# Kernel tuning notes

Hardware: AMD Instinct MI355X
Metric: run time of the kernel (lower is better)

## Reference

```python
import jax, jax.numpy as jnp
import numpy as np

BN_EPS = 1e-5


def _binarize_act(x):
    # sign(x) forward, clipped STE backward (grad passes where |x|<1)
    xc = jnp.clip(x, -1.0, 1.0)
    return xc + jax.lax.stop_gradient(jnp.sign(x) - xc)


def _binarize_weight(w):
    # XNOR/ReActNet: per-out-channel scale * sign(w); clipped-STE gradient
    scale = jax.lax.stop_gradient(jnp.mean(jnp.abs(w), axis=(1, 2, 3), keepdims=True))
    wc = jnp.clip(w, -1.0, 1.0)
    return wc + jax.lax.stop_gradient(scale * jnp.sign(w) - wc)


def setup_inputs() -> dict:
    key = jax.random.key(0)
    ks = jax.random.split(key, 8)
    B, C, H, W = 64, 64, 56, 56
    P = 64  # planes == inplanes (stride 1, no downsample)
    x = jax.random.normal(ks[0], (B, C, H, W), dtype=jnp.float32)
    bias0 = jnp.zeros((1, C, 1, 1), dtype=jnp.float32)
    w = jax.random.normal(ks[1], (P, C, 3, 3), dtype=jnp.float32) * 0.1
    gamma = jnp.ones((P,), dtype=jnp.float32)
    beta = jnp.zeros((P,), dtype=jnp.float32)
    run_mean = jax.random.normal(ks[2], (P,), dtype=jnp.float32) * 0.1
    run_var = jax.random.uniform(ks[3], (P,), dtype=jnp.float32, minval=0.5, maxval=1.5)
    bias1 = jnp.zeros((1, P, 1, 1), dtype=jnp.float32)
    alpha = jnp.full((P,), 0.25, dtype=jnp.float32)  # PReLU default init
    bias2 = jnp.zeros((1, P, 1, 1), dtype=jnp.float32)
    return {"x": x, "bias0": bias0, "w": w, "gamma": gamma, "beta": beta,
            "run_mean": run_mean, "run_var": run_var, "bias1": bias1,
            "alpha": alpha, "bias2": bias2}


def reference(x, bias0, w, gamma, beta, run_mean, run_var, bias1, alpha, bias2):
    residual = x
    out = x + bias0                      # move0 (LearnableBias)
    out = _binarize_act(out)             # BinAct: sign, clipped STE
    bw = _binarize_weight(w)             # BinConv weight binarization
    out = jax.lax.conv_general_dilated(
        out, bw, window_strides=(1, 1), padding=((1, 1), (1, 1)),
        dimension_numbers=("NCHW", "OIHW", "NCHW"))
    # BatchNorm2d (inference form with running stats)
    inv = gamma / jnp.sqrt(run_var + BN_EPS)
    out = out * inv[None, :, None, None] + (beta - run_mean * inv)[None, :, None, None]
    out = out + residual                 # residual add (downsample is None)
    out = out + bias1                    # move1
    a = alpha[None, :, None, None]
    out = jnp.where(out >= 0, out, a * out)  # PReLU
    out = out + bias2                    # move2
    return out
```

## Files before the change

### kernel.cpp

```cpp
#include <hip/hip_runtime.h>

typedef unsigned long long u64;

#define BATCH 64
#define CH    64
#define HH    56
#define WW    56
#define HW    3136
#define NBAND 14
#define NBLK  (BATCH * NBAND)

__global__ __launch_bounds__(256)
void fold_kernel(const float* __restrict__ w,
                 const float* __restrict__ gamma,
                 const float* __restrict__ beta,
                 const float* __restrict__ rmean,
                 const float* __restrict__ rvar,
                 const float* __restrict__ bias1,
                 const float* __restrict__ alpha,
                 const float* __restrict__ bias2,
                 u64* __restrict__ wbits,
                 float* __restrict__ kc,
                 float4* __restrict__ c4) {
    __shared__ float red[4];
    const int tid = threadIdx.x;
    const int lane = tid & 63;
    const int wv = tid >> 6;
    const int p = blockIdx.x;
    const float* wp = w + p * 576;

    float s = 0.f;
    for (int i = tid; i < 576; i += 256) s += fabsf(wp[i]);
#pragma unroll
    for (int off = 32; off > 0; off >>= 1) s += __shfl_down(s, off);
    if (lane == 0) red[wv] = s;
    __syncthreads();

    u64 m[9];
    if (wv == 0) {
#pragma unroll
        for (int t = 0; t < 9; ++t) {
            m[t] = __ballot(wp[lane * 9 + t] > 0.f);
            if (lane == 0) wbits[p * 10 + t] = m[t];
        }
        if (lane == 0) wbits[p * 10 + 9] = 0;
    }
    if (tid == 0) {
        float scale = (red[0] + red[1] + red[2] + red[3]) * (1.0f / 576.0f);
        float inv = gamma[p] * rsqrtf(rvar[p] + 1e-5f);
        float am = scale * inv;
        float bd = beta[p] - rmean[p] * inv + bias1[p];
        float pt[9];
#pragma unroll
        for (int t = 0; t < 9; ++t) pt[t] = (float)__popcll(m[t]);
        const float cL = pt[0] + pt[3] + pt[6];
        const float cR = pt[2] + pt[5] + pt[8];
        const float rT = pt[0] + pt[1] + pt[2];
        const float rB = pt[6] + pt[7] + pt[8];
        float Ci[3][3] = {
            {0.f, cL,                 cR},
            {rT,  rT + pt[3] + pt[6], rT + pt[5] + pt[8]},
            {rB,  rB + pt[0] + pt[3], rB + pt[2] + pt[5]}};
        float nv[3][3] = {{9, 6, 6}, {6, 4, 4}, {6, 4, 4}};
#pragma unroll
        for (int wc = 0; wc < 3; ++wc)
#pragma unroll
            for (int lc = 0; lc < 3; ++lc)
                kc[wc * 192 + lc * 64 + p] =
                    fmaf(am, 64.f * nv[wc][lc] + 2.f * Ci[wc][lc], bd);
        c4[p] = make_float4(-2.f * am, alpha[p], bias2[p], 0.f);
    }
}

__global__ __launch_bounds__(512, 6)
void fused_kernel(const float* __restrict__ x,
                  const float* __restrict__ bias0,
                  const u64* __restrict__ wbits,
                  const float* __restrict__ kc,
                  const float4* __restrict__ c4,
                  float* __restrict__ out) {
    __shared__ __align__(16) u64 Lsgn[6][58];
    __shared__ __align__(16) u64 wsm[64 * 10];
    __shared__ float kcsm[576];
    __shared__ float4 c4sm[64];

    const int tid = threadIdx.x;
    const int lane = tid & 63;
    const int wv = tid >> 6;

    for (int i = tid; i < 640; i += 512) wsm[i] = wbits[i];
    for (int i = tid; i < 576; i += 512) kcsm[i] = kc[i];
    if (tid < 64) c4sm[tid] = c4[tid];

    const int bid = blockIdx.x;
    const int wg = (bid & 7) * 112 + (bid >> 3);
    const int b = wg / NBAND;
    const int band = wg - b * NBAND;
    const int r0 = band * 4;

    if (wv < 6) {
        const int ir = r0 - 1 + wv;
        const bool rowok = (unsigned)ir < (unsigned)HH;
        u64 mine = 0;
        if (rowok) {
            const float* xp = x + ((size_t)(b * CH + lane)) * HW + ir * WW;
            const float bz = bias0[lane];
#pragma unroll
            for (int q = 0; q < 14; ++q) {
                float4 v = *(const float4*)(xp + q * 4);
                u64 m0 = __ballot(v.x + bz > 0.f);
                u64 m1 = __ballot(v.y + bz > 0.f);
                u64 m2 = __ballot(v.z + bz > 0.f);
                u64 m3 = __ballot(v.w + bz > 0.f);
                mine = (lane == q * 4 + 0) ? m0 : mine;
                mine = (lane == q * 4 + 1) ? m1 : mine;
                mine = (lane == q * 4 + 2) ? m2 : mine;
                mine = (lane == q * 4 + 3) ? m3 : mine;
            }
        }
        if (lane < WW) Lsgn[wv][1 + lane] = mine;
        else if (lane == 56) Lsgn[wv][0] = 0;
        else if (lane == 57) Lsgn[wv][57] = 0;
    }
    __syncthreads();

    const int rl = wv & 3;
    const int ph = (wv >> 2) << 5;
    const int h = r0 + rl;
    const int wcol = min(lane, WW - 1);
    const bool active = lane < WW;

    u64 a[9];
#pragma unroll
    for (int t = 0; t < 9; ++t)
        a[t] = Lsgn[rl + t / 3][wcol + t % 3];

    const int wclass = (h == 0) ? 1 : (h == HH - 1) ? 2 : 0;
    const int lclass = (wcol == 0) ? 1 : (lane == WW - 1) ? 2 : 0;
    const float* kp = kcsm + wclass * 192 + lclass * 64;

    const size_t xbase = (size_t)b * CH * HW + (size_t)h * WW + wcol;

#pragma unroll 4
    for (int i = 0; i < 32; ++i) {
        const int p = ph + i;
        const u64* wp = wsm + p * 10;
        unsigned int P = 0;
#pragma unroll
        for (int t = 0; t < 9; ++t) {
            u64 v = a[t] ^ wp[t];
            P += __popc((unsigned int)v);
            P += __popc((unsigned int)(v >> 32));
        }
        const float4 cc = c4sm[p];
        const float k = kp[p];
        const size_t off = xbase + (size_t)p * HW;
        const float res = x[off];
        float v = fmaf(cc.x, (float)P, k) + res;
        v = v >= 0.f ? v : cc.y * v;
        v += cc.z;
        if (active) out[off] = v;
    }
}

extern "C" void kernel_launch(void* const* d_in, const int* in_sizes, int n_in,
                              void* d_out, int out_size, void* d_ws, size_t ws_size,
                              hipStream_t stream) {
    const float* x     = (const float*)d_in[0];
    const float* bias0 = (const float*)d_in[1];
    const float* w     = (const float*)d_in[2];
    const float* gamma = (const float*)d_in[3];
    const float* beta  = (const float*)d_in[4];
    const float* rmean = (const float*)d_in[5];
    const float* rvar  = (const float*)d_in[6];
    const float* bias1 = (const float*)d_in[7];
    const float* alpha = (const float*)d_in[8];
    const float* bias2 = (const float*)d_in[9];
    float* out = (float*)d_out;

    char* ws = (char*)d_ws;
    u64* wbits = (u64*)ws;
    float* kc  = (float*)(ws + 5120);
    float4* c4 = (float4*)(ws + 8192);

    fold_kernel<<<64, 256, 0, stream>>>(
        w, gamma, beta, rmean, rvar, bias1, alpha, bias2, wbits, kc, c4);

    fused_kernel<<<NBLK, 512, 0, stream>>>(x, bias0, wbits, kc, c4, out);
}
```

Baseline: 48.38 us.

## Read packed weight table via scalar loads and prefetch residuals in a ring

Packs the weight sign bits and per-channel epilogue constants into one 12-word record per output channel. The fused kernel now reads that record straight from global memory through a wave-uniform pointer (readfirstlane), which allows scalar loads, instead of staging it in LDS. The residual x values are prefetched 8 channels ahead in a register ring, and the 32-iteration loop is fully unrolled with 32-bit offsets. This aims to cut LDS traffic and hide the latency of the residual loads, at the cost of higher register pressure.

Result: no change. 49.03 us (+1.4%).

```diff
diff --git a/kernel.cpp b/kernel.cpp
--- a/kernel.cpp
+++ b/kernel.cpp
@@ -1,6 +1,7 @@
 #include <hip/hip_runtime.h>
 
 typedef unsigned long long u64;
+typedef unsigned int u32;
 
 #define BATCH 64
 #define CH    64
@@ -19,9 +20,8 @@
                  const float* __restrict__ bias1,
                  const float* __restrict__ alpha,
                  const float* __restrict__ bias2,
-                 u64* __restrict__ wbits,
-                 float* __restrict__ kc,
-                 float4* __restrict__ c4) {
+                 u64* __restrict__ wtab,
+                 float* __restrict__ kc) {
     __shared__ float red[4];
     const int tid = threadIdx.x;
     const int lane = tid & 63;
@@ -36,61 +36,60 @@
     if (lane == 0) red[wv] = s;
     __syncthreads();
 
-    u64 m[9];
     if (wv == 0) {
+        u64 m[9];
 #pragma unroll
         for (int t = 0; t < 9; ++t) {
             m[t] = __ballot(wp[lane * 9 + t] > 0.f);
-            if (lane == 0) wbits[p * 10 + t] = m[t];
+            if (lane == 0) wtab[p * 12 + t] = m[t];
         }
-        if (lane == 0) wbits[p * 10 + 9] = 0;
-    }
-    if (tid == 0) {
-        float scale = (red[0] + red[1] + red[2] + red[3]) * (1.0f / 576.0f);
-        float inv = gamma[p] * rsqrtf(rvar[p] + 1e-5f);
-        float am = scale * inv;
-        float bd = beta[p] - rmean[p] * inv + bias1[p];
-        float pt[9];
-#pragma unroll
-        for (int t = 0; t < 9; ++t) pt[t] = (float)__popcll(m[t]);
-        const float cL = pt[0] + pt[3] + pt[6];
-        const float cR = pt[2] + pt[5] + pt[8];
-        const float rT = pt[0] + pt[1] + pt[2];
-        const float rB = pt[6] + pt[7] + pt[8];
-        float Ci[3][3] = {
-            {0.f, cL,                 cR},
-            {rT,  rT + pt[3] + pt[6], rT + pt[5] + pt[8]},
-            {rB,  rB + pt[0] + pt[3], rB + pt[2] + pt[5]}};
-        float nv[3][3] = {{9, 6, 6}, {6, 4, 4}, {6, 4, 4}};
-#pragma unroll
-        for (int wc = 0; wc < 3; ++wc)
-#pragma unroll
-            for (int lc = 0; lc < 3; ++lc)
-                kc[wc * 192 + lc * 64 + p] =
-                    fmaf(am, 64.f * nv[wc][lc] + 2.f * Ci[wc][lc], bd);
-        c4[p] = make_float4(-2.f * am, alpha[p], bias2[p], 0.f);
+        if (lane == 0) {
+            float scale = (red[0] + red[1] + red[2] + red[3]) * (1.0f / 576.0f);
+            float inv = gamma[p] * rsqrtf(rvar[p] + 1e-5f);
+            float am = scale * inv;
+            float bd = beta[p] - rmean[p] * inv + bias1[p];
+            float pt[9];
+#pragma unroll
+            for (int t = 0; t < 9; ++t) pt[t] = (float)__popcll(m[t]);
+            const float cL = pt[0] + pt[3] + pt[6];
+            const float cR = pt[2] + pt[5] + pt[8];
+            const float rT = pt[0] + pt[1] + pt[2];
+            const float rB = pt[6] + pt[7] + pt[8];
+            float Ci[3][3] = {
+                {0.f, cL,                 cR},
+                {rT,  rT + pt[3] + pt[6], rT + pt[5] + pt[8]},
+                {rB,  rB + pt[0] + pt[3], rB + pt[2] + pt[5]}};
+            float nv[3][3] = {{9, 6, 6}, {6, 4, 4}, {6, 4, 4}};
+#pragma unroll
+            for (int wc = 0; wc < 3; ++wc)
+#pragma unroll
+                for (int lc = 0; lc < 3; ++lc)
+                    kc[(wc * 3 + lc) * 64 + p] =
+                        fmaf(am, 64.f * nv[wc][lc] + 2.f * Ci[wc][lc], bd);
+            float* cf = (float*)(wtab + p * 12 + 9);
+            cf[0] = -2.f * am;
+            cf[1] = alpha[p];
+            cf[2] = bias2[p];
+            cf[3] = 0.f;
+            wtab[p * 12 + 11] = 0;
+        }
     }
 }
 
 __global__ __launch_bounds__(512, 6)
 void fused_kernel(const float* __restrict__ x,
                   const float* __restrict__ bias0,
-                  const u64* __restrict__ wbits,
+                  const u64* __restrict__ wtab,
                   const float* __restrict__ kc,
-                  const float4* __restrict__ c4,
                   float* __restrict__ out) {
     __shared__ __align__(16) u64 Lsgn[6][58];
-    __shared__ __align__(16) u64 wsm[64 * 10];
     __shared__ float kcsm[576];
-    __shared__ float4 c4sm[64];
 
     const int tid = threadIdx.x;
     const int lane = tid & 63;
     const int wv = tid >> 6;
 
-    for (int i = tid; i < 640; i += 512) wsm[i] = wbits[i];
     for (int i = tid; i < 576; i += 512) kcsm[i] = kc[i];
-    if (tid < 64) c4sm[tid] = c4[tid];
 
     const int bid = blockIdx.x;
     const int wg = (bid & 7) * 112 + (bid >> 3);
@@ -118,48 +117,60 @@
                 mine = (lane == q * 4 + 3) ? m3 : mine;
             }
         }
-        if (lane < WW) Lsgn[wv][1 + lane] = mine;
-        else if (lane == 56) Lsgn[wv][0] = 0;
-        else if (lane == 57) Lsgn[wv][57] = 0;
+        if (lane < WW)        Lsgn[wv][1 + lane] = mine;
+        else if (lane == 56)  Lsgn[wv][0] = 0;
+        else if (lane == 57)  Lsgn[wv][57] = 0;
     }
     __syncthreads();
 
     const int rl = wv & 3;
-    const int ph = (wv >> 2) << 5;
+    const int ph = __builtin_amdgcn_readfirstlane((wv >> 2) << 5);
     const int h = r0 + rl;
-    const int wcol = min(lane, WW - 1);
+    const int wl = min(lane, WW - 1);
     const bool active = lane < WW;
 
     u64 a[9];
 #pragma unroll
     for (int t = 0; t < 9; ++t)
-        a[t] = Lsgn[rl + t / 3][wcol + t % 3];
+        a[t] = Lsgn[rl + t / 3][wl + t % 3];
 
     const int wclass = (h == 0) ? 1 : (h == HH - 1) ? 2 : 0;
-    const int lclass = (wcol == 0) ? 1 : (lane == WW - 1) ? 2 : 0;
-    const float* kp = kcsm + wclass * 192 + lclass * 64;
-
-    const size_t xbase = (size_t)b * CH * HW + (size_t)h * WW + wcol;
-
-#pragma unroll 4
+    const int lclass = (lane == 0) ? 1 : (lane == WW - 1) ? 2 : 0;
+    const float* kp = kcsm + (wclass * 3 + lclass) * 64 + ph;
+
+    u32 off = (u32)(b * CH * HW + h * WW + wl) + (u32)ph * HW;
+    const u64* wp = wtab + ph * 12;
+
+    float res[8];
+#pragma unroll
+    for (int j = 0; j < 8; ++j) res[j] = x[off + (u32)j * HW];
+
+#pragma unroll
     for (int i = 0; i < 32; ++i) {
-        const int p = ph + i;
-        const u64* wp = wsm + p * 10;
-        unsigned int P = 0;
-#pragma unroll
-        for (int t = 0; t < 9; ++t) {
-            u64 v = a[t] ^ wp[t];
-            P += __popc((unsigned int)v);
-            P += __popc((unsigned int)(v >> 32));
-        }
-        const float4 cc = c4sm[p];
-        const float k = kp[p];
-        const size_t off = xbase + (size_t)p * HW;
-        const float res = x[off];
-        float v = fmaf(cc.x, (float)P, k) + res;
-        v = v >= 0.f ? v : cc.y * v;
-        v += cc.z;
-        if (active) out[off] = v;
+        const float rcur = res[i & 7];
+        if (i + 8 < 32) res[i & 7] = x[off + 8u * HW];
+
+        u32 P = 0;
+        u64 v;
+        v = a[0] ^ wp[0]; P += __popc((u32)v); P += __popc((u32)(v >> 32));
+        v = a[1] ^ wp[1]; P += __popc((u32)v); P += __popc((u32)(v >> 32));
+        v = a[2] ^ wp[2]; P += __popc((u32)v); P += __popc((u32)(v >> 32));
+        v = a[3] ^ wp[3]; P += __popc((u32)v); P += __popc((u32)(v >> 32));
+        v = a[4] ^ wp[4]; P += __popc((u32)v); P += __popc((u32)(v >> 32));
+        v = a[5] ^ wp[5]; P += __popc((u32)v); P += __popc((u32)(v >> 32));
+        v = a[6] ^ wp[6]; P += __popc((u32)v); P += __popc((u32)(v >> 32));
+        v = a[7] ^ wp[7]; P += __popc((u32)v); P += __popc((u32)(v >> 32));
+        v = a[8] ^ wp[8]; P += __popc((u32)v); P += __popc((u32)(v >> 32));
+
+        const float* cf = (const float*)(wp + 9);
+        const float k = kp[i];
+        float o = fmaf(cf[0], (float)P, k) + rcur;
+        o = o >= 0.f ? o : cf[1] * o;
+        o += cf[2];
+        if (active) out[off] = o;
+
+        off += HW;
+        wp += 12;
     }
 }
 
@@ -179,12 +190,11 @@
     float* out = (float*)d_out;
 
     char* ws = (char*)d_ws;
-    u64* wbits = (u64*)ws;
-    float* kc  = (float*)(ws + 5120);
-    float4* c4 = (float4*)(ws + 8192);
+    u64* wtab = (u64*)ws;
+    float* kc = (float*)(ws + 6144);
 
     fold_kernel<<<64, 256, 0, stream>>>(
-        w, gamma, beta, rmean, rvar, bias1, alpha, bias2, wbits, kc, c4);
-
-    fused_kernel<<<NBLK, 512, 0, stream>>>(x, bias0, wbits, kc, c4, out);
+        w, gamma, beta, rmean, rvar, bias1, alpha, bias2, wtab, kc);
+
+    fused_kernel<<<NBLK, 512, 0, stream>>>(x, bias0, wtab, kc, out);
 }
```
